# Kernel tuning notes

Hardware: AMD Instinct MI355X
Metric: run time of the kernel (lower is better)

Reference implementation:

```python
import jax, jax.numpy as jnp
import numpy as np

B, T, C, H = 2, 2048, 1024, 16
NS, NL, STEP = 3, 1, 8            # n_s_token, n_l_token, online_step
NPF = NS + NL                      # tokens per frame
CHUNK = STEP * NPF                 # online chunk size = 32
D = C // H


def _build_causal_mask():
    # Faithful port of the buffer construction in __init__ (host-side numpy).
    m = np.tril(np.ones((T, T), dtype=np.float32))
    step = np.zeros((T, T), dtype=np.float32)
    for i in range(0, T, CHUNK):
        step[i:i + CHUNK, i:i + CHUNK] = 1.0
        for j in range(i, i + CHUNK, NPF):
            m[j + NS:j + NPF, :] = 0.0
            m[:, j + NS:j + NPF] = 0.0
    return jnp.asarray(((m + step) == 0.0))[None, None]  # (1,1,T,T) bool


def setup_inputs() -> dict:
    key = jax.random.key(0)
    ks = jax.random.split(key, 10)
    sc = 0.02
    return {
        "x": jax.random.normal(ks[0], (B, T, C), dtype=jnp.float32),
        "dynamic_mask": jax.random.randint(ks[1], (B, 1, T, T), 0, 2).astype(bool),
        "causal_mask": _build_causal_mask(),
        "Wq": jax.random.normal(ks[2], (C, C), dtype=jnp.float32) * sc,
        "bq": jnp.zeros((C,), dtype=jnp.float32),
        "Wk": jax.random.normal(ks[3], (C, C), dtype=jnp.float32) * sc,
        "bk": jnp.zeros((C,), dtype=jnp.float32),
        "Wv": jax.random.normal(ks[4], (C, C), dtype=jnp.float32) * sc,
        "bv": jnp.zeros((C,), dtype=jnp.float32),
        "Wo": jax.random.normal(ks[5], (C, C), dtype=jnp.float32) * sc,
        "bo": jnp.zeros((C,), dtype=jnp.float32),
    }


def reference(x, dynamic_mask, causal_mask, Wq, bq, Wk, bk, Wv, bv, Wo, bo):
    Bb, Tt, Cc = x.shape
    scale = jnp.asarray(D, x.dtype) ** -0.5
    # nn.Linear: y = x @ W.T + b ; split heads -> (B,H,T,D)
    q = (x @ Wq.T + bq).reshape(Bb, Tt, H, D).transpose(0, 2, 1, 3)
    k = (x @ Wk.T + bk).reshape(Bb, Tt, H, D).transpose(0, 2, 1, 3)
    v = (x @ Wv.T + bv).reshape(Bb, Tt, H, D).transpose(0, 2, 1, 3)
    att = jnp.einsum('bhqd,bhkd->bhqk', q, k) * scale       # (B,H,T,T)
    neg_inf = jnp.asarray(-jnp.inf, att.dtype)
    att = jnp.where(causal_mask, neg_inf, att)
    att = jnp.where(dynamic_mask, neg_inf, att)
    att = jax.nn.softmax(att, axis=-1)                      # attn_drop is identity (eval)
    y = jnp.einsum('bhqk,bhkd->bhqd', att, v)
    y = y.transpose(0, 2, 1, 3).reshape(Bb, Tt, Cc)
    return y @ Wo.T + bo                                    # resid_drop is identity (eval)
```

## Files before the change

### kernel.cpp

```cpp
#include <hip/hip_runtime.h>

#define TSEQ 2048
#define NHEAD 16
#define DHEAD 64
#define CDIM 1024
#define BATCH 2

typedef __attribute__((ext_vector_type(8))) short bfx8;
typedef __attribute__((ext_vector_type(4))) short bfx4;
typedef __attribute__((ext_vector_type(4))) float f32x4;

__device__ __forceinline__ unsigned short f2bf(float f) {
  unsigned u = __builtin_bit_cast(unsigned, f);
  u += 0x7fffu + ((u >> 16) & 1u);
  return (unsigned short)(u >> 16);
}

__device__ __forceinline__ unsigned cvtpk(float lo, float hi) {
  unsigned r;
  asm("v_cvt_pk_bf16_f32 %0, %1, %2" : "=v"(r) : "v"(lo), "v"(hi));
  return r;
}

__device__ __forceinline__ float max3f(float a, float b, float c) {
  float d;
  asm("v_max3_f32 %0, %1, %2, %3" : "=v"(d) : "v"(a), "v"(b), "v"(c));
  return d;
}

__device__ __forceinline__ void gload16(const void* g, void* l) {
  __builtin_amdgcn_global_load_lds(
      (const __attribute__((address_space(1))) unsigned*)g,
      (__attribute__((address_space(3))) unsigned*)l, 16, 0, 0);
}

__global__ __launch_bounds__(256) void convert_all(
    const float* __restrict__ x,
    const float* __restrict__ wq, const float* __restrict__ wk,
    const float* __restrict__ wv, const float* __restrict__ wo,
    short* __restrict__ xb, short* __restrict__ wall) {
  const int y = blockIdx.y;
  const float* src;
  short* dst;
  int n;
  if (y == 0) { src = x; dst = xb; n = (BATCH * TSEQ * CDIM) / 4; }
  else {
    src = (y == 1) ? wq : (y == 2) ? wk : (y == 3) ? wv : wo;
    dst = wall + (size_t)(y - 1) * CDIM * CDIM;
    n = (CDIM * CDIM) / 4;
  }
  const int i = blockIdx.x * 256 + threadIdx.x;
  if (i < n) {
    const float4 v = ((const float4*)src)[i];
    bfx4 o;
    o[0] = (short)f2bf(v.x); o[1] = (short)f2bf(v.y);
    o[2] = (short)f2bf(v.z); o[3] = (short)f2bf(v.w);
    ((bfx4*)dst)[i] = o;
  }
}

__global__ __launch_bounds__(256) void maskpack(
    const unsigned char* __restrict__ dyn,
    const unsigned char* __restrict__ causal,
    unsigned long long* __restrict__ pm) {
  const bool mbyte = (causal[32] != 0);
  const int wave = threadIdx.x >> 6, lane = threadIdx.x & 63;
  const int gid = blockIdx.x * 4 + wave;
  const int tile = gid & 31;
  const int q = (gid >> 5) & (TSEQ - 1);
  const int b = gid >> 16;
  const int g = lane >> 4, blk = (lane >> 2) & 3, r = lane & 3;
  const int k = tile * 64 + blk * 16 + g * 4 + r;
  const size_t off = ((size_t)b * TSEQ + q) * TSEQ + k;
  const bool dm = mbyte ? (dyn[off] != 0) : (((const int*)dyn)[off] != 0);
  const bool qok = (q & 3) != 3;
  const bool al =
      (((k >> 5) == (q >> 5)) || ((k <= q) && qok && (r != 3))) && !dm;
  const unsigned long long bal = __ballot(!al);
  if (lane == 0) pm[gid] = bal;
}

__global__ __launch_bounds__(256) void gemm_qkv(
    const short* __restrict__ A, const short* __restrict__ Ball,
    const float* __restrict__ bias0, const float* __restrict__ bias1,
    const float* __restrict__ bias2,
    short* __restrict__ Oq, short* __restrict__ Ok, short* __restrict__ VT) {
  __shared__ char arena[35072];
  const int tid = threadIdx.x;
  const int w = tid >> 6, lane = tid & 63;
  const int lq = lane & 15, g = lane >> 4;
  const int wr = w >> 1, wc = w & 1;
  const int m0 = blockIdx.x * 128, n0 = blockIdx.y * 128;
  const int which = blockIdx.z;
  const short* B = Ball + (size_t)which * CDIM * CDIM;
#define ASB(bi) ((short*)(arena + (bi) * 8192))
#define BSB(bi) ((short*)(arena + 16384 + (bi) * 8192))
#define GS(bi, kt)                                                             \
  {                                                                            \
    _Pragma("unroll") for (int ph = 0; ph < 2; ++ph) {                         \
      const int c = ph * 256 + tid;                                            \
      gload16(A + (size_t)(m0 + (c >> 2)) * CDIM + (kt) * 32 + (c & 3) * 8,    \
              ASB(bi) + (ph * 256 + w * 64) * 8);                              \
      gload16(B + (size_t)(n0 + (c >> 2)) * CDIM + (kt) * 32 + (c & 3) * 8,    \
              BSB(bi) + (ph * 256 + w * 64) * 8);                              \
    }                                                                          \
  }
  GS(0, 0);
  __syncthreads();
  f32x4 acc[4][4] = {};
#pragma unroll 2
  for (int kt = 0; kt < CDIM / 32; ++kt) {
    const int bi = kt & 1;
    if (kt + 1 < CDIM / 32) GS(bi ^ 1, kt + 1);
    bfx8 af[4], bfr[4];
#pragma unroll
    for (int i = 0; i < 4; ++i)
      af[i] = *(const bfx8*)&ASB(bi)[(wr * 64 + i * 16 + lq) * 32 + g * 8];
#pragma unroll
    for (int i = 0; i < 4; ++i)
      bfr[i] = *(const bfx8*)&BSB(bi)[(wc * 64 + i * 16 + lq) * 32 + g * 8];
#pragma unroll
    for (int i = 0; i < 4; ++i)
#pragma unroll
      for (int j = 0; j < 4; ++j)
        acc[i][j] = __builtin_amdgcn_mfma_f32_16x16x32_bf16(af[i], bfr[j],
                                                            acc[i][j], 0, 0, 0);
    __syncthreads();
  }
#undef GS
  const float* bias = (which == 0) ? bias0 : (which == 1) ? bias1 : bias2;
  const float scale = (which == 0) ? 0.18033688011112042f : 1.0f;
  short* tile = (short*)arena;
  const int rs = (which == 2) ? 137 : 136;
#pragma unroll
  for (int i = 0; i < 4; ++i)
#pragma unroll
    for (int j = 0; j < 4; ++j) {
      const int col = wc * 64 + j * 16 + lq;
      const float bb = bias[n0 + col];
#pragma unroll
      for (int r = 0; r < 4; ++r) {
        const int row = wr * 64 + i * 16 + g * 4 + r;
        tile[row * rs + col] = (short)f2bf((acc[i][j][r] + bb) * scale);
      }
    }
  __syncthreads();
  const int b_ = m0 >> 11, t0 = m0 & (TSEQ - 1);
  if (which == 2) {
#pragma unroll
    for (int it = 0; it < 8; ++it) {
      const int id = it * 256 + tid;
      const int tseg = id & 15, d128 = id >> 4;
      const int h = (n0 >> 6) + (d128 >> 6), d = d128 & 63;
      bfx8 o;
#pragma unroll
      for (int j = 0; j < 8; ++j) o[j] = tile[(tseg * 8 + j) * 137 + d128];
      *(bfx8*)&VT[(((size_t)b_ * NHEAD + h) * DHEAD + d) * TSEQ + t0 +
                  tseg * 8] = o;
    }
  } else {
    short* O = (which == 0) ? Oq : Ok;
#pragma unroll
    for (int it = 0; it < 8; ++it) {
      const int id = it * 256 + tid;
      const int m = id >> 4, c16 = id & 15;
      const int h = (n0 >> 6) + (c16 >> 3), d0 = (c16 & 7) * 8;
      *(bfx8*)&O[(((size_t)b_ * NHEAD + h) * TSEQ + t0 + m) * DHEAD + d0] =
          *(const bfx8*)&tile[m * 136 + c16 * 8];
    }
  }
}

__global__ __launch_bounds__(256) void gemm_out(
    const short* __restrict__ A, const short* __restrict__ B,
    const float* __restrict__ bias, float* __restrict__ Of) {
  __shared__ char arena[24576];
  const int tid = threadIdx.x;
  const int w = tid >> 6, lane = tid & 63;
  const int lq = lane & 15, g = lane >> 4;
  const int wr = w >> 1, wc = w & 1;
  const int m0 = blockIdx.x * 64, n0 = blockIdx.y * 128;
#define ASB(bi) ((short*)(arena + (bi) * 4096))
#define BSB(bi) ((short*)(arena + 8192 + (bi) * 8192))
#define GS(bi, kt)                                                             \
  {                                                                            \
    gload16(A + (size_t)(m0 + (tid >> 2)) * CDIM + (kt) * 32 + (tid & 3) * 8,  \
            ASB(bi) + (w * 64) * 8);                                           \
    _Pragma("unroll") for (int ph = 0; ph < 2; ++ph) {                         \
      const int c = ph * 256 + tid;                                            \
      gload16(B + (size_t)(n0 + (c >> 2)) * CDIM + (kt) * 32 + (c & 3) * 8,    \
              BSB(bi) + (ph * 256 + w * 64) * 8);                              \
    }                                                                          \
  }
  GS(0, 0);
  __syncthreads();
  f32x4 acc[2][4] = {};
#pragma unroll 2
  for (int kt = 0; kt < CDIM / 32; ++kt) {
    const int bi = kt & 1;
    if (kt + 1 < CDIM / 32) GS(bi ^ 1, kt + 1);
    bfx8 af[2], bfr[4];
#pragma unroll
    for (int i = 0; i < 2; ++i)
      af[i] = *(const bfx8*)&ASB(bi)[(wr * 32 + i * 16 + lq) * 32 + g * 8];
#pragma unroll
    for (int j = 0; j < 4; ++j)
      bfr[j] = *(const bfx8*)&BSB(bi)[(wc * 64 + j * 16 + lq) * 32 + g * 8];
#pragma unroll
    for (int i = 0; i < 2; ++i)
#pragma unroll
      for (int j = 0; j < 4; ++j)
        acc[i][j] = __builtin_amdgcn_mfma_f32_16x16x32_bf16(af[i], bfr[j],
                                                            acc[i][j], 0, 0, 0);
    __syncthreads();
  }
#undef GS
#undef ASB
#undef BSB
#pragma unroll
  for (int i = 0; i < 2; ++i)
#pragma unroll
    for (int j = 0; j < 4; ++j) {
      const int col = n0 + wc * 64 + j * 16 + lq;
      const float bb = bias[col];
#pragma unroll
      for (int r = 0; r < 4; ++r) {
        const int row = m0 + wr * 32 + i * 16 + g * 4 + r;
        Of[(size_t)row * CDIM + col] = acc[i][j][r] + bb;
      }
    }
}

struct QPhase {
  bfx8 qf0, qf1;
  f32x4 acc[4];
  float m, l;
  const unsigned short* pmr;
};

__device__ __forceinline__ void attn_half(QPhase& S, const char* kbuf,
                                          const char* vbuf, short* Pw,
                                          unsigned mb, int hf, int sw, int lq,
                                          int g) {
  f32x4 st[2] = {};
  __builtin_amdgcn_s_setprio(1);
#pragma unroll
  for (int b2 = 0; b2 < 2; ++b2) {
    const int rowb = ((hf * 2 + b2) * 16 + lq) * 128;
    const bfx8 kf0 = *(const bfx8*)&kbuf[rowb + ((g * 16) ^ sw)];
    const bfx8 kf1 = *(const bfx8*)&kbuf[rowb + ((64 + g * 16) ^ sw)];
    st[b2] =
        __builtin_amdgcn_mfma_f32_16x16x32_bf16(kf0, S.qf0, st[b2], 0, 0, 0);
    st[b2] =
        __builtin_amdgcn_mfma_f32_16x16x32_bf16(kf1, S.qf1, st[b2], 0, 0, 0);
  }
  __builtin_amdgcn_s_setprio(0);
  float s8[8];
#pragma unroll
  for (int idx = 0; idx < 8; ++idx)
    s8[idx] = ((mb >> idx) & 1u) ? -3.0e38f : st[idx >> 2][idx & 3];
  const float t0 = max3f(s8[0], s8[1], s8[2]);
  const float t1 = max3f(s8[3], s8[4], s8[5]);
  const float pmax = max3f(t0, t1, fmaxf(s8[6], s8[7]));
  if (!__all(pmax - S.m <= 8.f)) {
    float smax = fmaxf(pmax, __shfl_xor(pmax, 16));
    smax = fmaxf(smax, __shfl_xor(smax, 32));
    const float mnew = fmaxf(S.m, smax);
    const float fac = __builtin_amdgcn_exp2f(S.m - mnew);
    S.l *= fac;
    float fr[4];
#pragma unroll
    for (int r = 0; r < 4; ++r) fr[r] = __shfl(fac, g * 4 + r);
#pragma unroll
    for (int dc = 0; dc < 4; ++dc) {
      S.acc[dc][0] *= fr[0]; S.acc[dc][1] *= fr[1];
      S.acc[dc][2] *= fr[2]; S.acc[dc][3] *= fr[3];
    }
    S.m = mnew;
  }
  float psum = 0.f;
#pragma unroll
  for (int idx = 0; idx < 8; ++idx) {
    const float e = __builtin_amdgcn_exp2f(s8[idx] - S.m);
    s8[idx] = e;
    psum += e;
  }
  S.l += psum;
#pragma unroll
  for (int b2 = 0; b2 < 2; ++b2) {
    uint2 u;
    u.x = cvtpk(s8[b2 * 4 + 0], s8[b2 * 4 + 1]);
    u.y = cvtpk(s8[b2 * 4 + 2], s8[b2 * 4 + 3]);
    *(uint2*)&Pw[lq * 40 + b2 * 16 + g * 4] = u;
  }
  __builtin_amdgcn_wave_barrier();
  const bfx8 pa = *(const bfx8*)&Pw[lq * 40 + g * 8];
  __builtin_amdgcn_wave_barrier();
  __builtin_amdgcn_s_setprio(1);
#pragma unroll
  for (int dc = 0; dc < 4; ++dc) {
    const bfx8 vf = *(const bfx8*)&vbuf[(dc * 16 + lq) * 128 +
                                        ((hf * 64 + g * 16) ^ sw)];
    S.acc[dc] =
        __builtin_amdgcn_mfma_f32_16x16x32_bf16(pa, vf, S.acc[dc], 0, 0, 0);
  }
  __builtin_amdgcn_s_setprio(0);
}

__global__ __launch_bounds__(512, 4) void attn(
    const short* __restrict__ Q, const short* __restrict__ K,
    const short* __restrict__ VT, const unsigned short* __restrict__ pm,
    short* __restrict__ Y) {
  __shared__ char arena[43008];
  const int tid = threadIdx.x;
  const int w = tid >> 6, lane = tid & 63;
  const int hf = w >> 2, ws = w & 3;
  const int lq = lane & 15, g = lane >> 4;
  const int bh = blockIdx.y, b = bh >> 4, h = bh & 15;
  const int tlo = blockIdx.x, thi = 31 - tlo;
  const short* Qb = Q + (size_t)bh * TSEQ * DHEAD;
  const short* Kb = K + (size_t)bh * TSEQ * DHEAD;
  const short* Vb = VT + (size_t)bh * DHEAD * TSEQ;

  QPhase lo, hi;
  {
    const int qlo = tlo * 64 + ws * 16 + lq;
    const int qhi = thi * 64 + ws * 16 + lq;
    lo.qf0 = *(const bfx8*)(Qb + (size_t)qlo * DHEAD + g * 8);
    lo.qf1 = *(const bfx8*)(Qb + (size_t)qlo * DHEAD + 32 + g * 8);
    hi.qf0 = *(const bfx8*)(Qb + (size_t)qhi * DHEAD + g * 8);
    hi.qf1 = *(const bfx8*)(Qb + (size_t)qhi * DHEAD + 32 + g * 8);
#pragma unroll
    for (int dc = 0; dc < 4; ++dc) { lo.acc[dc] = f32x4{}; hi.acc[dc] = f32x4{}; }
    lo.m = -1e30f; lo.l = 0.f; hi.m = -1e30f; hi.l = 0.f;
    lo.pmr = pm + ((size_t)(b * TSEQ + qlo) << 7) + g;
    hi.pmr = pm + ((size_t)(b * TSEQ + qhi) << 7) + g;
  }

  const int sl = lane >> 3, sc = lane & 7;
  const int ssw = (sc ^ sl) * 8;
  const int sw = (lq & 7) << 4;
  short* Pw = (short*)(arena + 32768 + w * 1280);

#define STAGE(bufn, k0s)                                                      \
  {                                                                           \
    gload16(Kb + (size_t)((k0s) + w * 8 + sl) * DHEAD + ssw,                  \
            arena + (bufn) * 16384 + w * 1024);                               \
    gload16(Vb + (size_t)(w * 8 + sl) * TSEQ + (k0s) + ssw,                   \
            arena + (bufn) * 16384 + 8192 + w * 1024);                        \
  }

#define PHASE(t, BUF)                                                         \
  {                                                                           \
    const unsigned pmh = hi.pmr[(t) << 2];                                    \
    const unsigned pml = ((t) <= tlo) ? (unsigned)lo.pmr[(t) << 2] : 0u;      \
    __builtin_amdgcn_sched_barrier(0);                                        \
    if ((t) < thi) STAGE((BUF) ^ 1, ((t) + 1) * 64);                          \
    const char* kbuf_ = arena + (BUF) * 16384;                                \
    const char* vbuf_ = kbuf_ + 8192;                                         \
    attn_half(hi, kbuf_, vbuf_, Pw, (pmh >> (hf * 8)) & 0xffu, hf, sw, lq, g);\
    if ((t) <= tlo)                                                           \
      attn_half(lo, kbuf_, vbuf_, Pw, (pml >> (hf * 8)) & 0xffu, hf, sw, lq,  \
                g);                                                           \
    __syncthreads();                                                          \
  }

  STAGE(0, 0);
  __syncthreads();

  int t = 0;
  for (; t + 1 <= thi; t += 2) {
    PHASE(t, 0);
    PHASE(t + 1, 1);
  }
  if (t <= thi) PHASE(t, 0);
#undef PHASE
#undef STAGE

  float* exA = (float*)arena;
  float2* exM = (float2*)(arena + 32768);
  if (hf == 1) {
#pragma unroll
    for (int ph = 0; ph < 2; ++ph) {
      QPhase& S = ph ? hi : lo;
      float* a = exA + (ws * 2 + ph) * 1024;
#pragma unroll
      for (int dc = 0; dc < 4; ++dc)
        *(f32x4*)&a[lane * 16 + dc * 4] = S.acc[dc];
      exM[(ws * 2 + ph) * 64 + lane] = float2{S.m, S.l};
    }
  }
  __syncthreads();
  if (hf == 0) {
#pragma unroll
    for (int ph = 0; ph < 2; ++ph) {
      QPhase& S = ph ? hi : lo;
      const float* a = exA + (ws * 2 + ph) * 1024;
      const float2 mlB = exM[(ws * 2 + ph) * 64 + lane];
      const float ms = fmaxf(S.m, mlB.x);
      const float fA = __builtin_amdgcn_exp2f(S.m - ms);
      const float fB = __builtin_amdgcn_exp2f(mlB.x - ms);
      float lr = S.l * fA + mlB.y * fB;
      lr += __shfl_xor(lr, 16);
      lr += __shfl_xor(lr, 32);
      float frA[4], frB[4], li[4];
#pragma unroll
      for (int r = 0; r < 4; ++r) {
        frA[r] = __shfl(fA, g * 4 + r);
        frB[r] = __shfl(fB, g * 4 + r);
        const float lv = __shfl(lr, g * 4 + r);
        li[r] = lv > 0.f ? 1.f / lv : 0.f;
      }
      const int q0 = (ph ? thi : tlo) * 64 + ws * 16;
#pragma unroll
      for (int dc = 0; dc < 4; ++dc) {
        const f32x4 ab = *(const f32x4*)&a[lane * 16 + dc * 4];
#pragma unroll
        for (int r = 0; r < 4; ++r) {
          const int t2 = q0 + g * 4 + r;
          Y[((size_t)b * TSEQ + t2) * CDIM + h * DHEAD + dc * 16 + lq] =
              (short)f2bf((S.acc[dc][r] * frA[r] + ab[r] * frB[r]) * li[r]);
        }
      }
    }
  }
}

extern "C" void kernel_launch(void* const* d_in, const int* in_sizes, int n_in,
                              void* d_out, int out_size, void* d_ws,
                              size_t ws_size, hipStream_t stream) {
  const float* x = (const float*)d_in[0];
  const unsigned char* dyn = (const unsigned char*)d_in[1];
  const unsigned char* causal = (const unsigned char*)d_in[2];
  const float* Wq = (const float*)d_in[3];
  const float* bq = (const float*)d_in[4];
  const float* Wk = (const float*)d_in[5];
  const float* bk = (const float*)d_in[6];
  const float* Wv = (const float*)d_in[7];
  const float* bv = (const float*)d_in[8];
  const float* Wo = (const float*)d_in[9];
  const float* bo = (const float*)d_in[10];

  char* ws = (char*)d_ws;
  const size_t MB8 = 8ull * 1024 * 1024;
  short* xb = (short*)(ws + 0 * MB8);
  short* wall = (short*)(ws + 1 * MB8);
  short* Qb = (short*)(ws + 2 * MB8);
  short* Kb = (short*)(ws + 3 * MB8);
  short* VTb = (short*)(ws + 5 * MB8);
  short* Yb = (short*)(ws + 6 * MB8);
  unsigned long long* pmask = (unsigned long long*)(ws + 7 * MB8);

  convert_all<<<dim3(4096, 5), 256, 0, stream>>>(x, Wq, Wk, Wv, Wo, xb, wall);
  maskpack<<<dim3(32768), 256, 0, stream>>>(dyn, causal, pmask);
  gemm_qkv<<<dim3(32, 8, 3), 256, 0, stream>>>(xb, wall, bq, bk, bv, Qb, Kb,
                                               VTb);
  attn<<<dim3(16, 32), 512, 0, stream>>>(Qb, Kb, VTb,
                                         (const unsigned short*)pmask, Yb);
  gemm_out<<<dim3(64, 8), 256, 0, stream>>>(Yb, wall + 3 * CDIM * CDIM, bo,
                                            (float*)d_out);
}
```

Before: 126.9 us.

## Merge prep kernels and remap block IDs for XCD-aware L2 locality

Fuses the float-to-bf16 conversion kernel and the mask-packing kernel into one launch, removing one kernel launch. Flattens the grids of gemm_qkv, attn and gemm_out to 1D and remaps block IDs so blocks that land on the same XCD (round-robin by bid&7) share A/B tiles or the same heads. The aim is better per-XCD L2 reuse on the MI355X's chiplet layout. The remapping adds a little index arithmetic and assumes round-robin dispatch across the eight XCDs.

```diff
diff --git a/kernel.cpp b/kernel.cpp
--- a/kernel.cpp
+++ b/kernel.cpp
@@ -34,50 +34,51 @@
       (__attribute__((address_space(3))) unsigned*)l, 16, 0, 0);
 }
 
-__global__ __launch_bounds__(256) void convert_all(
+__global__ __launch_bounds__(256) void prep(
     const float* __restrict__ x,
     const float* __restrict__ wq, const float* __restrict__ wk,
     const float* __restrict__ wv, const float* __restrict__ wo,
-    short* __restrict__ xb, short* __restrict__ wall) {
-  const int y = blockIdx.y;
-  const float* src;
-  short* dst;
-  int n;
-  if (y == 0) { src = x; dst = xb; n = (BATCH * TSEQ * CDIM) / 4; }
-  else {
-    src = (y == 1) ? wq : (y == 2) ? wk : (y == 3) ? wv : wo;
-    dst = wall + (size_t)(y - 1) * CDIM * CDIM;
-    n = (CDIM * CDIM) / 4;
-  }
-  const int i = blockIdx.x * 256 + threadIdx.x;
-  if (i < n) {
-    const float4 v = ((const float4*)src)[i];
-    bfx4 o;
-    o[0] = (short)f2bf(v.x); o[1] = (short)f2bf(v.y);
-    o[2] = (short)f2bf(v.z); o[3] = (short)f2bf(v.w);
-    ((bfx4*)dst)[i] = o;
-  }
-}
-
-__global__ __launch_bounds__(256) void maskpack(
+    short* __restrict__ xb, short* __restrict__ wall,
     const unsigned char* __restrict__ dyn,
     const unsigned char* __restrict__ causal,
     unsigned long long* __restrict__ pm) {
-  const bool mbyte = (causal[32] != 0);
-  const int wave = threadIdx.x >> 6, lane = threadIdx.x & 63;
-  const int gid = blockIdx.x * 4 + wave;
-  const int tile = gid & 31;
-  const int q = (gid >> 5) & (TSEQ - 1);
-  const int b = gid >> 16;
-  const int g = lane >> 4, blk = (lane >> 2) & 3, r = lane & 3;
-  const int k = tile * 64 + blk * 16 + g * 4 + r;
-  const size_t off = ((size_t)b * TSEQ + q) * TSEQ + k;
-  const bool dm = mbyte ? (dyn[off] != 0) : (((const int*)dyn)[off] != 0);
-  const bool qok = (q & 3) != 3;
-  const bool al =
-      (((k >> 5) == (q >> 5)) || ((k <= q) && qok && (r != 3))) && !dm;
-  const unsigned long long bal = __ballot(!al);
-  if (lane == 0) pm[gid] = bal;
+  const int bid = blockIdx.x;
+  if (bid < 20480) {
+    const int y = bid >> 12;
+    const float* src;
+    short* dst;
+    int n;
+    if (y == 0) { src = x; dst = xb; n = (BATCH * TSEQ * CDIM) / 4; }
+    else {
+      src = (y == 1) ? wq : (y == 2) ? wk : (y == 3) ? wv : wo;
+      dst = wall + (size_t)(y - 1) * CDIM * CDIM;
+      n = (CDIM * CDIM) / 4;
+    }
+    const int i = (bid & 4095) * 256 + threadIdx.x;
+    if (i < n) {
+      const float4 v = ((const float4*)src)[i];
+      bfx4 o;
+      o[0] = (short)f2bf(v.x); o[1] = (short)f2bf(v.y);
+      o[2] = (short)f2bf(v.z); o[3] = (short)f2bf(v.w);
+      ((bfx4*)dst)[i] = o;
+    }
+  } else {
+    const bool mbyte = (causal[32] != 0);
+    const int wave = threadIdx.x >> 6, lane = threadIdx.x & 63;
+    const int gid = (bid - 20480) * 4 + wave;
+    const int tile = gid & 31;
+    const int q = (gid >> 5) & (TSEQ - 1);
+    const int b = gid >> 16;
+    const int g = lane >> 4, blk = (lane >> 2) & 3, r = lane & 3;
+    const int k = tile * 64 + blk * 16 + g * 4 + r;
+    const size_t off = ((size_t)b * TSEQ + q) * TSEQ + k;
+    const bool dm = mbyte ? (dyn[off] != 0) : (((const int*)dyn)[off] != 0);
+    const bool qok = (q & 3) != 3;
+    const bool al =
+        (((k >> 5) == (q >> 5)) || ((k <= q) && qok && (r != 3))) && !dm;
+    const unsigned long long bal = __ballot(!al);
+    if (lane == 0) pm[gid] = bal;
+  }
 }
 
 __global__ __launch_bounds__(256) void gemm_qkv(
@@ -86,12 +87,16 @@
     const float* __restrict__ bias2,
     short* __restrict__ Oq, short* __restrict__ Ok, short* __restrict__ VT) {
   __shared__ char arena[35072];
+  const int bid = blockIdx.x;
+  const int xcd = bid & 7, local = bid >> 3;
+  const int m_idx = (xcd >> 1) * 8 + (local & 7);
+  const int nz = (xcd & 1) * 12 + (local >> 3);
+  const int which = nz >> 3, n_idx = nz & 7;
   const int tid = threadIdx.x;
   const int w = tid >> 6, lane = tid & 63;
   const int lq = lane & 15, g = lane >> 4;
   const int wr = w >> 1, wc = w & 1;
-  const int m0 = blockIdx.x * 128, n0 = blockIdx.y * 128;
-  const int which = blockIdx.z;
+  const int m0 = m_idx * 128, n0 = n_idx * 128;
   const short* B = Ball + (size_t)which * CDIM * CDIM;
 #define ASB(bi) ((short*)(arena + (bi) * 8192))
 #define BSB(bi) ((short*)(arena + 16384 + (bi) * 8192))
@@ -175,11 +180,15 @@
     const short* __restrict__ A, const short* __restrict__ B,
     const float* __restrict__ bias, float* __restrict__ Of) {
   __shared__ char arena[24576];
+  const int bid = blockIdx.x;
+  const int xcd = bid & 7, local = bid >> 3;
+  const int m_idx = (xcd >> 1) * 16 + (local & 15);
+  const int n_idx = (xcd & 1) * 4 + (local >> 4);
   const int tid = threadIdx.x;
   const int w = tid >> 6, lane = tid & 63;
   const int lq = lane & 15, g = lane >> 4;
   const int wr = w >> 1, wc = w & 1;
-  const int m0 = blockIdx.x * 64, n0 = blockIdx.y * 128;
+  const int m0 = m_idx * 64, n0 = n_idx * 128;
 #define ASB(bi) ((short*)(arena + (bi) * 4096))
 #define BSB(bi) ((short*)(arena + 8192 + (bi) * 8192))
 #define GS(bi, kt)                                                             \
@@ -312,12 +321,15 @@
     const short* __restrict__ VT, const unsigned short* __restrict__ pm,
     short* __restrict__ Y) {
   __shared__ char arena[43008];
+  const int bid = blockIdx.x;
+  const int local = bid >> 3;
+  const int bh = (bid & 7) * 4 + (local >> 4);
+  const int tlo = local & 15, thi = 31 - tlo;
   const int tid = threadIdx.x;
   const int w = tid >> 6, lane = tid & 63;
   const int hf = w >> 2, ws = w & 3;
   const int lq = lane & 15, g = lane >> 4;
-  const int bh = blockIdx.y, b = bh >> 4, h = bh & 15;
-  const int tlo = blockIdx.x, thi = 31 - tlo;
+  const int b = bh >> 4, h = bh & 15;
   const short* Qb = Q + (size_t)bh * TSEQ * DHEAD;
   const short* Kb = K + (size_t)bh * TSEQ * DHEAD;
   const short* Vb = VT + (size_t)bh * DHEAD * TSEQ;
@@ -451,12 +463,11 @@
   short* Yb = (short*)(ws + 6 * MB8);
   unsigned long long* pmask = (unsigned long long*)(ws + 7 * MB8);
 
-  convert_all<<<dim3(4096, 5), 256, 0, stream>>>(x, Wq, Wk, Wv, Wo, xb, wall);
-  maskpack<<<dim3(32768), 256, 0, stream>>>(dyn, causal, pmask);
-  gemm_qkv<<<dim3(32, 8, 3), 256, 0, stream>>>(xb, wall, bq, bk, bv, Qb, Kb,
-                                               VTb);
-  attn<<<dim3(16, 32), 512, 0, stream>>>(Qb, Kb, VTb,
-                                         (const unsigned short*)pmask, Yb);
-  gemm_out<<<dim3(64, 8), 256, 0, stream>>>(Yb, wall + 3 * CDIM * CDIM, bo,
-                                            (float*)d_out);
-}
+  prep<<<dim3(53248), 256, 0, stream>>>(x, Wq, Wk, Wv, Wo, xb, wall, dyn,
+                                        causal, pmask);
+  gemm_qkv<<<dim3(768), 256, 0, stream>>>(xb, wall, bq, bk, bv, Qb, Kb, VTb);
+  attn<<<dim3(512), 512, 0, stream>>>(Qb, Kb, VTb,
+                                      (const unsigned short*)pmask, Yb);
+  gemm_out<<<dim3(512), 256, 0, stream>>>(Yb, wall + 3 * CDIM * CDIM, bo,
+                                          (float*)d_out);
+}
```

Result: faster. 122.5 us, median of 2 (-3.4%).
